# Optimization experiments

Hardware: AMD Instinct MI355X
Metric: run time of the kernel (lower is better)

Reference implementation:

```python
import jax, jax.numpy as jnp
import numpy as np

B, S, HID = 2, 2048, 4096
NUM_HEADS, NUM_KV_HEADS, HEAD_DIM = 32, 8, 128
KV_SIZE = HID * NUM_KV_HEADS // NUM_HEADS  # 1024


def setup_inputs() -> dict:
    key = jax.random.key(0)
    ks = jax.random.split(key, 5)
    x = jax.random.normal(ks[0], (B, S, HID), dtype=jnp.float32)
    wq = jax.random.normal(ks[1], (HID, HID), dtype=jnp.float32) * 0.02
    wk = jax.random.normal(ks[2], (HID, KV_SIZE), dtype=jnp.float32) * 0.02
    wv = jax.random.normal(ks[3], (HID, KV_SIZE), dtype=jnp.float32) * 0.02
    wo = jax.random.normal(ks[4], (KV_SIZE, HID), dtype=jnp.float32) * 0.02
    return {"x": x, "wq": wq, "wk": wk, "wv": wv, "wo": wo}


def reference(x, wq, wk, wv, wo):
    b, s, _ = x.shape
    g = NUM_HEADS // NUM_KV_HEADS  # num_head_groups
    q = x @ wq  # [b, s, hid]
    k = x @ wk  # [b, s, kv_size]
    v = x @ wv  # [b, s, kv_size]
    # 'b s (h d) -> b h s d' with h = num_heads
    q = q.reshape(b, s, NUM_HEADS, HEAD_DIM).transpose(0, 2, 1, 3)
    # 'b s (h d) -> b h d s' with h = num_kv_heads
    k = k.reshape(b, s, NUM_KV_HEADS, HEAD_DIM).transpose(0, 2, 3, 1)
    # 'b s (h d) -> b h s d'
    v = v.reshape(b, s, NUM_KV_HEADS, HEAD_DIM).transpose(0, 2, 1, 3)
    # 'b (h g) s d -> b g h s d' with g = num_head_groups, h = num_kv_heads
    q = q.reshape(b, NUM_KV_HEADS, g, s, HEAD_DIM).transpose(0, 2, 1, 3, 4)
    # NOTE: faithful to source - g is contracted (summed) here, it does not
    # appear in the output subscripts.
    scores = jnp.einsum('bghqd,bhdk->bhqk', q, k) / jnp.sqrt(
        jnp.asarray(HEAD_DIM, dtype=x.dtype))
    scores = jax.nn.softmax(scores, axis=-1)
    values = jnp.einsum('bhqk,bhkd->bhqd', scores, v)  # [b, h_kv, s, d]
    values = values.transpose(0, 2, 1, 3).reshape(b, s, KV_SIZE)
    return values @ wo  # [b, s, hid]
```

## Files before the change

kernel.cpp:

```cpp
#include <hip/hip_runtime.h>
#include <stdint.h>

#define S 2048
#define HID 4096
#define NKV 8
#define HD 128
#define KV 1024
#define BATCH 2
#define NQKV 3072
#define MROWS 4096

typedef __attribute__((ext_vector_type(4))) float f32x4;
typedef __attribute__((ext_vector_type(8))) __bf16 bf16x8;
typedef __attribute__((ext_vector_type(8))) unsigned short ushort8;
typedef __attribute__((ext_vector_type(4))) unsigned short ushort4_t;
typedef __attribute__((ext_vector_type(4))) float float4_t;

__device__ __forceinline__ unsigned short f2bf(float f) {
    unsigned int u = __builtin_bit_cast(unsigned int, f);
    u += 0x7fffu + ((u >> 16) & 1u);
    return (unsigned short)(u >> 16);
}
__device__ __forceinline__ float bf2f(unsigned short s) {
    unsigned int u = ((unsigned int)s) << 16;
    return __builtin_bit_cast(float, u);
}

__device__ __forceinline__ void gl2lds16(const void* g, void* l) {
    __builtin_amdgcn_global_load_lds(
        (const __attribute__((address_space(1))) void*)(uintptr_t)(g),
        (__attribute__((address_space(3))) void*)(uintptr_t)(l),
        16, 0, 0);
}

__global__ __launch_bounds__(256) void castx_kernel(const float* __restrict__ x,
                                                    unsigned short* __restrict__ xb) {
    int i = (blockIdx.x * 256 + threadIdx.x) * 4;
    float4_t v = *(const float4_t*)&x[i];
    ushort4_t o;
    o.x = f2bf(v.x); o.y = f2bf(v.y); o.z = f2bf(v.z); o.w = f2bf(v.w);
    *(ushort4_t*)&xb[i] = o;
}

__global__ __launch_bounds__(256) void wcat_kernel(const float* __restrict__ wq,
                                                   const float* __restrict__ wk,
                                                   const float* __restrict__ wv,
                                                   unsigned short* __restrict__ WcatT) {
    __shared__ float T[64 * 65];
    const int tid = threadIdx.x;
    const int k0 = blockIdx.x * 64;
    const int n0 = blockIdx.y * 64;
    const float scale = 0.088388347648318447f;
#pragma unroll
    for (int i = 0; i < 16; i++) {
        int kl = (tid >> 6) + i * 4;
        int nl = tid & 63;
        int k = k0 + kl, n = n0 + nl;
        float v;
        if (n < KV) {
            int kvh = n >> 7, d = n & 127;
            const float* p = wq + (size_t)k * HID + kvh * 512 + d;
            v = (p[0] + p[128] + p[256] + p[384]) * scale;
        } else if (n < 2048) {
            v = wk[(size_t)k * KV + (n - KV)];
        } else {
            v = wv[(size_t)k * KV + (n - 2048)];
        }
        T[kl * 65 + nl] = v;
    }
    __syncthreads();
#pragma unroll
    for (int i = 0; i < 16; i++) {
        int nl = (tid >> 6) + i * 4;
        int kl = tid & 63;
        WcatT[(size_t)(n0 + nl) * HID + k0 + kl] = f2bf(T[kl * 65 + nl]);
    }
}

__global__ __launch_bounds__(256) void wot_kernel(const float* __restrict__ wo,
                                                  unsigned short* __restrict__ woT) {
    __shared__ float T[64 * 65];
    const int tid = threadIdx.x;
    const int k0 = blockIdx.x * 64;
    const int n0 = blockIdx.y * 64;
#pragma unroll
    for (int i = 0; i < 16; i++) {
        int kl = (tid >> 6) + i * 4, nl = tid & 63;
        T[kl * 65 + nl] = wo[(size_t)(k0 + kl) * HID + n0 + nl];
    }
    __syncthreads();
#pragma unroll
    for (int i = 0; i < 16; i++) {
        int nl = (tid >> 6) + i * 4, kl = tid & 63;
        woT[(size_t)(n0 + nl) * KV + k0 + kl] = f2bf(T[kl * 65 + nl]);
    }
}

#define SBAR() __builtin_amdgcn_s_barrier()
#define SCHED0() __builtin_amdgcn_sched_barrier(0)
#define WAITV6() asm volatile("s_waitcnt vmcnt(6)")

template <int OUT_BF16>
__global__ __launch_bounds__(512, 2) void gemm_bt8(const unsigned short* __restrict__ A,
                                                   const unsigned short* __restrict__ Bt,
                                                   void* __restrict__ Cv,
                                                   int M, int N, int K) {
    __shared__ unsigned short As[2][2][8192];
    __shared__ unsigned short Bs[2][2][8192];
    const int tid = threadIdx.x;
    const int lane = tid & 63, wave = tid >> 6;
    const int lm = lane & 15, quad = lane >> 4;
    const int wm = wave >> 2;
    const int wn = wave & 3;
    const int wnh = wn >> 1;
    const int wnb = (wn & 1) * 4;

    const int nbx = gridDim.x;
    const int id = blockIdx.y * nbx + blockIdx.x;
    const int cpx = (nbx * gridDim.y) >> 3;
    const int sid = (id & 7) * cpx + (id >> 3);
    const int m0 = (sid / nbx) * 256;
    const int n0 = (sid % nbx) * 256;

    size_t so0, so1;
    {
#pragma unroll
        for (int i = 0; i < 2; i++) {
            int p = i * 512 + tid;
            int ps = p ^ (((p >> 5) & 1) << 1);
            int s = ps >> 6, w = ps & 63;
            int row = ((s >> 1) << 4) + (w >> 2);
            int kc = ((s & 1) << 5) + ((w & 3) << 3);
            size_t off = (size_t)row * K + kc;
            if (i == 0) so0 = off; else so1 = off;
        }
    }
    const unsigned short* Agb = A + (size_t)m0 * K;
    const unsigned short* Bgb = Bt + (size_t)n0 * K;
    const size_t hK = (size_t)128 * K;

#define STLO(G, L) gl2lds16((G) + so0, (L) + (size_t)tid * 8)
#define STHI(G, L) gl2lds16((G) + so1, (L) + (size_t)(512 + tid) * 8)

    const int roff = lm * 32 + ((quad << 3) ^ (((lm >> 3) & 1) << 4));

#define LDA(mi, kk, BUF) a[(mi) & 3][kk] = *(const bf16x8*)&As[BUF][wm][(((mi) * 2 + (kk)) << 9) + roff]
#define LDB(ni, kk, BUF) b[ni][kk] = *(const bf16x8*)&Bs[BUF][wnh][(((wnb + (ni)) * 2 + (kk)) << 9) + roff]
#define RD_A_LO(BUF) { LDA(0,0,BUF); LDA(0,1,BUF); LDA(1,0,BUF); LDA(1,1,BUF); LDA(2,0,BUF); LDA(2,1,BUF); LDA(3,0,BUF); LDA(3,1,BUF); }
#define RD_A_HI(BUF) { LDA(4,0,BUF); LDA(4,1,BUF); LDA(5,0,BUF); LDA(5,1,BUF); LDA(6,0,BUF); LDA(6,1,BUF); LDA(7,0,BUF); LDA(7,1,BUF); }
#define RD_B_LO(BUF) { LDB(0,0,BUF); LDB(0,1,BUF); LDB(1,0,BUF); LDB(1,1,BUF); }
#define RD_B_HI(BUF) { LDB(2,0,BUF); LDB(2,1,BUF); LDB(3,0,BUF); LDB(3,1,BUF); }
#define MFMA_Q(MB, NB) do { \
    __builtin_amdgcn_s_setprio(1); \
    _Pragma("unroll") for (int i_ = 0; i_ < 4; i_++) \
    _Pragma("unroll") for (int j_ = 0; j_ < 2; j_++) \
    _Pragma("unroll") for (int k_ = 0; k_ < 2; k_++) \
        acc[(MB) + i_][(NB) + j_] = __builtin_amdgcn_mfma_f32_16x16x32_bf16( \
            a[i_][k_], b[(NB) + j_][k_], acc[(MB) + i_][(NB) + j_], 0, 0, 0); \
    __builtin_amdgcn_s_setprio(0); \
} while (0)

    f32x4 acc[8][4] = {};
    bf16x8 a[4][2], b[4][2];

    const int KT = K >> 6;
    const int NT = KT >> 1;

    STLO(Agb, &As[0][0][0]); STLO(Agb + hK, &As[0][1][0]);
    STHI(Agb, &As[0][0][0]); STHI(Agb + hK, &As[0][1][0]);
    STLO(Bgb, &Bs[0][0][0]); STLO(Bgb + hK, &Bs[0][1][0]);
    STHI(Bgb, &Bs[0][0][0]); STHI(Bgb + hK, &Bs[0][1][0]);
    STLO(Agb + 64, &As[1][0][0]); STLO(Agb + hK + 64, &As[1][1][0]);
    STLO(Bgb + 64, &Bs[1][0][0]); STLO(Bgb + hK + 64, &Bs[1][1][0]);
    STHI(Bgb + 64, &Bs[1][0][0]); STHI(Bgb + hK + 64, &Bs[1][1][0]);
    WAITV6();
    SCHED0();
    SBAR();

    for (int t = 0; t < NT; ++t) {
        const size_t k1 = (size_t)(2 * t + 1) * 64;
        int t2i = 2 * t + 2; if (t2i >= KT) t2i = KT - 1;
        int t3i = 2 * t + 3; if (t3i >= KT) t3i = KT - 1;
        const size_t k2 = (size_t)t2i * 64, k3 = (size_t)t3i * 64;

        RD_A_LO(0); RD_B_LO(0);
        STHI(Agb + k1, &As[1][0][0]); STHI(Agb + hK + k1, &As[1][1][0]);
        SCHED0(); SBAR(); MFMA_Q(0, 0); SBAR();

        RD_B_HI(0);
        STLO(Agb + k2, &As[0][0][0]); STLO(Agb + hK + k2, &As[0][1][0]);
        SCHED0(); SBAR(); MFMA_Q(0, 2); SBAR();

        RD_A_HI(0);
        STLO(Bgb + k2, &Bs[0][0][0]); STLO(Bgb + hK + k2, &Bs[0][1][0]);
        SCHED0(); SBAR(); MFMA_Q(4, 2); SBAR();

        STHI(Bgb + k2, &Bs[0][0][0]); STHI(Bgb + hK + k2, &Bs[0][1][0]);
        SCHED0(); SBAR(); MFMA_Q(4, 0);
        WAITV6();
        SCHED0();
        SBAR();

        RD_A_LO(1); RD_B_LO(1);
        STHI(Agb + k2, &As[0][0][0]); STHI(Agb + hK + k2, &As[0][1][0]);
        SCHED0(); SBAR(); MFMA_Q(0, 0); SBAR();

        RD_B_HI(1);
        STLO(Agb + k3, &As[1][0][0]); STLO(Agb + hK + k3, &As[1][1][0]);
        SCHED0(); SBAR(); MFMA_Q(0, 2); SBAR();

        RD_A_HI(1);
        STLO(Bgb + k3, &Bs[1][0][0]); STLO(Bgb + hK + k3, &Bs[1][1][0]);
        SCHED0(); SBAR(); MFMA_Q(4, 2); SBAR();

        STHI(Bgb + k3, &Bs[1][0][0]); STHI(Bgb + hK + k3, &Bs[1][1][0]);
        SCHED0(); SBAR(); MFMA_Q(4, 0);
        WAITV6();
        SCHED0();
        SBAR();
    }

    const int crow0 = m0 + wm * 128 + quad * 4;
    const int ccol0 = n0 + wn * 64 + lm;
#pragma unroll
    for (int mi = 0; mi < 8; mi++)
#pragma unroll
        for (int ni = 0; ni < 4; ni++)
#pragma unroll
            for (int r = 0; r < 4; r++) {
                const int row = crow0 + mi * 16 + r;
                const int col = ccol0 + ni * 16;
                if (OUT_BF16)
                    ((unsigned short*)Cv)[(size_t)row * N + col] = f2bf(acc[mi][ni][r]);
                else
                    ((float*)Cv)[(size_t)row * N + col] = acc[mi][ni][r];
            }
#undef LDA
#undef LDB
#undef RD_A_LO
#undef RD_A_HI
#undef RD_B_LO
#undef RD_B_HI
#undef MFMA_Q
#undef STLO
#undef STHI
}

__global__ __launch_bounds__(256) void vt_kernel(const unsigned short* __restrict__ QKV,
                                                 unsigned short* __restrict__ Vt) {
    __shared__ unsigned short T[128 * 136];
    const int tid = threadIdx.x;
    const int st = blockIdx.x;
    const int bh = blockIdx.y;
    const int b = bh >> 3, h = bh & 7;
#pragma unroll
    for (int it = 0; it < 8; it++) {
        int chunk = tid + it * 256;
        int s = chunk >> 4, cc = chunk & 15;
        ushort8 v = *(const ushort8*)&QKV[(size_t)(b * S + st * 128 + s) * NQKV + 2048 + h * HD + cc * 8];
        *(ushort8*)&T[s * 136 + cc * 8] = v;
    }
    __syncthreads();
#pragma unroll
    for (int it = 0; it < 8; it++) {
        int chunk = tid + it * 256;
        int d = chunk >> 4, scc = chunk & 15;
        ushort8 o;
#pragma unroll
        for (int j = 0; j < 8; j++) o[j] = T[(scc * 8 + j) * 136 + d];
        *(ushort8*)&Vt[(size_t)((b * NKV + h) * HD + d) * S + st * 128 + scc * 8] = o;
    }
}

__global__ __launch_bounds__(256, 2) void attn_kernel(const unsigned short* __restrict__ QKV,
                                                      const unsigned short* __restrict__ Vt,
                                                      unsigned short* __restrict__ Oout) {
    __shared__ unsigned short Ks[64 * 128];
    __shared__ unsigned short Vs[128 * 64];
    __shared__ unsigned short Ps[64 * 64];
    const int tid = threadIdx.x;
    const int lane = tid & 63, wave = tid >> 6;
    const int lm = lane & 15, quad = lane >> 4;
    const int sw = lm & 7;
    const int h = blockIdx.x;
    const int qt = blockIdx.y;
    const int b = blockIdx.z;
    const int qrow0 = qt * 64 + wave * 16;

    bf16x8 qf[4];
#pragma unroll
    for (int ks = 0; ks < 4; ks++) {
        size_t off = (size_t)(b * S + qrow0 + lm) * NQKV + h * HD + ks * 32 + quad * 8;
        qf[ks] = *(const bf16x8*)&QKV[off];
    }

    float lsum[4] = {};
    f32x4 oacc[8] = {};

    const int krow = tid >> 2, kc4 = tid & 3;
    const int vrow = tid >> 1, vc2 = tid & 1;
    const unsigned short* Kg0 = QKV + (size_t)(b * S) * NQKV + KV + h * HD + kc4 * 32;
    const unsigned short* Vg0 = Vt + (size_t)((b * NKV + h) * HD + vrow) * S + vc2 * 32;

    ushort8 kreg[4], vreg[4];
    {
        const unsigned short* kg = Kg0 + (size_t)krow * NQKV;
        const unsigned short* vg = Vg0;
#pragma unroll
        for (int j = 0; j < 4; j++) kreg[j] = *(const ushort8*)(kg + j * 8);
#pragma unroll
        for (int j = 0; j < 4; j++) vreg[j] = *(const ushort8*)(vg + j * 8);
    }

    for (int kt = 0; kt < 32; kt++) {
        __syncthreads();
#pragma unroll
        for (int j = 0; j < 4; j++)
            *(ushort8*)&Ks[krow * 128 + ((kc4 * 4 + j) ^ (krow & 7)) * 8] = kreg[j];
#pragma unroll
        for (int j = 0; j < 4; j++)
            *(ushort8*)&Vs[vrow * 64 + ((vc2 * 4 + j) ^ (vrow & 7)) * 8] = vreg[j];
        __syncthreads();
        if (kt < 31) {
            const unsigned short* kg = Kg0 + (size_t)((kt + 1) * 64 + krow) * NQKV;
            const unsigned short* vg = Vg0 + (kt + 1) * 64;
#pragma unroll
            for (int j = 0; j < 4; j++) kreg[j] = *(const ushort8*)(kg + j * 8);
#pragma unroll
            for (int j = 0; j < 4; j++) vreg[j] = *(const ushort8*)(vg + j * 8);
        }

        f32x4 sc[4] = {};
#pragma unroll
        for (int ks = 0; ks < 4; ks++)
#pragma unroll
            for (int ct = 0; ct < 4; ct++) {
                bf16x8 kf = *(const bf16x8*)&Ks[(ct * 16 + lm) * 128 + ((ks * 4 + quad) ^ sw) * 8];
                sc[ct] = __builtin_amdgcn_mfma_f32_16x16x32_bf16(qf[ks], kf, sc[ct], 0, 0, 0);
            }

#pragma unroll
        for (int ct = 0; ct < 4; ct++)
#pragma unroll
            for (int r = 0; r < 4; r++) {
                float p = __expf(fminf(sc[ct][r], 60.f));
                unsigned short pb = f2bf(p);
                lsum[r] += bf2f(pb);
                int prow = wave * 16 + quad * 4 + r;
                int pcol = ct * 16 + lm;
                Ps[prow * 64 + (((pcol >> 3) ^ (prow & 7)) * 8) + (pcol & 7)] = pb;
            }

#pragma unroll
        for (int ks = 0; ks < 2; ks++) {
            bf16x8 af = *(const bf16x8*)&Ps[(wave * 16 + lm) * 64 + ((ks * 4 + quad) ^ sw) * 8];
#pragma unroll
            for (int dt = 0; dt < 8; dt++) {
                bf16x8 vf = *(const bf16x8*)&Vs[(dt * 16 + lm) * 64 + ((ks * 4 + quad) ^ sw) * 8];
                oacc[dt] = __builtin_amdgcn_mfma_f32_16x16x32_bf16(af, vf, oacc[dt], 0, 0, 0);
            }
        }
    }

#pragma unroll
    for (int r = 0; r < 4; r++) {
        float v = lsum[r];
        v += __shfl_xor(v, 8);
        v += __shfl_xor(v, 4);
        v += __shfl_xor(v, 2);
        v += __shfl_xor(v, 1);
        lsum[r] = v;
    }
#pragma unroll
    for (int dt = 0; dt < 8; dt++)
#pragma unroll
        for (int r = 0; r < 4; r++) {
            int row = b * S + qt * 64 + wave * 16 + quad * 4 + r;
            int col = h * HD + dt * 16 + lm;
            Oout[(size_t)row * KV + col] = f2bf(oacc[dt][r] / lsum[r]);
        }
}

extern "C" void kernel_launch(void* const* d_in, const int* in_sizes, int n_in,
                              void* d_out, int out_size, void* d_ws, size_t ws_size,
                              hipStream_t stream) {
    (void)in_sizes; (void)n_in; (void)out_size; (void)ws_size;
    const float* x  = (const float*)d_in[0];
    const float* wq = (const float*)d_in[1];
    const float* wk = (const float*)d_in[2];
    const float* wv = (const float*)d_in[3];
    const float* wo = (const float*)d_in[4];
    float* out = (float*)d_out;
    char* ws = (char*)d_ws;

    unsigned short* xb    = (unsigned short*)(ws);
    unsigned short* WcatT = (unsigned short*)(ws + 33554432);
    unsigned short* woT   = (unsigned short*)(ws + 33554432 + 25165824);
    unsigned short* QKV   = (unsigned short*)(ws + 67108864);
    unsigned short* Vt    = (unsigned short*)(ws);
    unsigned short* AttnO = (unsigned short*)(ws + 8388608);

    castx_kernel<<<16384, 256, 0, stream>>>(x, xb);
    wcat_kernel<<<dim3(64, 48), 256, 0, stream>>>(wq, wk, wv, WcatT);
    wot_kernel<<<dim3(16, 64), 256, 0, stream>>>(wo, woT);
    gemm_bt8<1><<<dim3(NQKV / 256, MROWS / 256), 512, 0, stream>>>(xb, WcatT, QKV, MROWS, NQKV, HID);
    vt_kernel<<<dim3(16, 16), 256, 0, stream>>>(QKV, Vt);
    attn_kernel<<<dim3(NKV, 32, BATCH), 256, 0, stream>>>(QKV, Vt, AttnO);
    gemm_bt8<0><<<dim3(HID / 256, MROWS / 256), 512, 0, stream>>>(AttnO, woT, out, MROWS, HID, KV);
}
```

Baseline: 427.1 us.

## Fuse V transpose into QKV GEMM epilogue and prefetch LDS fragments earlier

The QKV GEMM gains an output mode that writes the V columns directly in transposed [b,h,d,s] layout as bf16. When the workspace is large enough this replaces the separate vt_kernel launch and its extra read/write of V. The GEMM main loop is also reorganised: B fragments are split into two register sets and the A/B LDS reads for the next quarter are issued before the barrier or after the MFMAs, so LDS latency overlaps compute. The transposed stores are 8-byte strided writes, which may coalesce poorly, and the extra fragment registers raise register pressure.

```diff
diff --git a/kernel.cpp b/kernel.cpp
--- a/kernel.cpp
+++ b/kernel.cpp
@@ -100,10 +100,11 @@
 #define SCHED0() __builtin_amdgcn_sched_barrier(0)
 #define WAITV6() asm volatile("s_waitcnt vmcnt(6)")
 
-template <int OUT_BF16>
+template <int OUT_MODE>
 __global__ __launch_bounds__(512, 2) void gemm_bt8(const unsigned short* __restrict__ A,
                                                    const unsigned short* __restrict__ Bt,
                                                    void* __restrict__ Cv,
+                                                   unsigned short* __restrict__ VtT,
                                                    int M, int N, int K) {
     __shared__ unsigned short As[2][2][8192];
     __shared__ unsigned short Bs[2][2][8192];
@@ -144,24 +145,26 @@
 
     const int roff = lm * 32 + ((quad << 3) ^ (((lm >> 3) & 1) << 4));
 
-#define LDA(mi, kk, BUF) a[(mi) & 3][kk] = *(const bf16x8*)&As[BUF][wm][(((mi) * 2 + (kk)) << 9) + roff]
-#define LDB(ni, kk, BUF) b[ni][kk] = *(const bf16x8*)&Bs[BUF][wnh][(((wnb + (ni)) * 2 + (kk)) << 9) + roff]
-#define RD_A_LO(BUF) { LDA(0,0,BUF); LDA(0,1,BUF); LDA(1,0,BUF); LDA(1,1,BUF); LDA(2,0,BUF); LDA(2,1,BUF); LDA(3,0,BUF); LDA(3,1,BUF); }
-#define RD_A_HI(BUF) { LDA(4,0,BUF); LDA(4,1,BUF); LDA(5,0,BUF); LDA(5,1,BUF); LDA(6,0,BUF); LDA(6,1,BUF); LDA(7,0,BUF); LDA(7,1,BUF); }
-#define RD_B_LO(BUF) { LDB(0,0,BUF); LDB(0,1,BUF); LDB(1,0,BUF); LDB(1,1,BUF); }
-#define RD_B_HI(BUF) { LDB(2,0,BUF); LDB(2,1,BUF); LDB(3,0,BUF); LDB(3,1,BUF); }
-#define MFMA_Q(MB, NB) do { \
+#define RA(mi, kk, BUF) (*(const bf16x8*)&As[BUF][wm][(((mi) * 2 + (kk)) << 9) + roff])
+#define RB(ni, kk, BUF) (*(const bf16x8*)&Bs[BUF][wnh][(((wnb + (ni)) * 2 + (kk)) << 9) + roff])
+#define RD_A_LO_K0(BUF) { a[0][0]=RA(0,0,BUF); a[1][0]=RA(1,0,BUF); a[2][0]=RA(2,0,BUF); a[3][0]=RA(3,0,BUF); }
+#define RD_A_LO_K1(BUF) { a[0][1]=RA(0,1,BUF); a[1][1]=RA(1,1,BUF); a[2][1]=RA(2,1,BUF); a[3][1]=RA(3,1,BUF); }
+#define RD_A_HI(BUF)    { a[0][0]=RA(4,0,BUF); a[0][1]=RA(4,1,BUF); a[1][0]=RA(5,0,BUF); a[1][1]=RA(5,1,BUF); \
+                          a[2][0]=RA(6,0,BUF); a[2][1]=RA(6,1,BUF); a[3][0]=RA(7,0,BUF); a[3][1]=RA(7,1,BUF); }
+#define RD_BN(BUF) { bn[0][0]=RB(0,0,BUF); bn[0][1]=RB(0,1,BUF); bn[1][0]=RB(1,0,BUF); bn[1][1]=RB(1,1,BUF); }
+#define RD_BH(BUF) { bh[0][0]=RB(2,0,BUF); bh[0][1]=RB(2,1,BUF); bh[1][0]=RB(3,0,BUF); bh[1][1]=RB(3,1,BUF); }
+#define MFMA_Q(MB, NB, BB) do { \
     __builtin_amdgcn_s_setprio(1); \
     _Pragma("unroll") for (int i_ = 0; i_ < 4; i_++) \
     _Pragma("unroll") for (int j_ = 0; j_ < 2; j_++) \
     _Pragma("unroll") for (int k_ = 0; k_ < 2; k_++) \
         acc[(MB) + i_][(NB) + j_] = __builtin_amdgcn_mfma_f32_16x16x32_bf16( \
-            a[i_][k_], b[(NB) + j_][k_], acc[(MB) + i_][(NB) + j_], 0, 0, 0); \
+            a[i_][k_], BB[j_][k_], acc[(MB) + i_][(NB) + j_], 0, 0, 0); \
     __builtin_amdgcn_s_setprio(0); \
 } while (0)
 
     f32x4 acc[8][4] = {};
-    bf16x8 a[4][2], b[4][2];
+    bf16x8 a[4][2], bn[2][2], bh[2][2];
 
     const int KT = K >> 6;
     const int NT = KT >> 1;
@@ -175,6 +178,7 @@
     STHI(Bgb + 64, &Bs[1][0][0]); STHI(Bgb + hK + 64, &Bs[1][1][0]);
     WAITV6();
     SCHED0();
+    RD_A_LO_K0(0); RD_BN(0);
     SBAR();
 
     for (int t = 0; t < NT; ++t) {
@@ -183,64 +187,78 @@
         int t3i = 2 * t + 3; if (t3i >= KT) t3i = KT - 1;
         const size_t k2 = (size_t)t2i * 64, k3 = (size_t)t3i * 64;
 
-        RD_A_LO(0); RD_B_LO(0);
+        RD_A_LO_K1(0); RD_BH(0);
         STHI(Agb + k1, &As[1][0][0]); STHI(Agb + hK + k1, &As[1][1][0]);
-        SCHED0(); SBAR(); MFMA_Q(0, 0); SBAR();
-
-        RD_B_HI(0);
+        SCHED0(); SBAR(); MFMA_Q(0, 0, bn); SBAR();
+
         STLO(Agb + k2, &As[0][0][0]); STLO(Agb + hK + k2, &As[0][1][0]);
-        SCHED0(); SBAR(); MFMA_Q(0, 2); SBAR();
-
-        RD_A_HI(0);
+        SCHED0(); SBAR(); MFMA_Q(0, 2, bh); RD_A_HI(0); SBAR();
+
         STLO(Bgb + k2, &Bs[0][0][0]); STLO(Bgb + hK + k2, &Bs[0][1][0]);
-        SCHED0(); SBAR(); MFMA_Q(4, 2); SBAR();
+        SCHED0(); SBAR(); MFMA_Q(4, 2, bh); SBAR();
 
         STHI(Bgb + k2, &Bs[0][0][0]); STHI(Bgb + hK + k2, &Bs[0][1][0]);
-        SCHED0(); SBAR(); MFMA_Q(4, 0);
-        WAITV6();
-        SCHED0();
+        SCHED0(); SBAR(); MFMA_Q(4, 0, bn);
+        WAITV6(); SCHED0();
+        RD_A_LO_K0(1); RD_BN(1);
         SBAR();
 
-        RD_A_LO(1); RD_B_LO(1);
+        RD_A_LO_K1(1); RD_BH(1);
         STHI(Agb + k2, &As[0][0][0]); STHI(Agb + hK + k2, &As[0][1][0]);
-        SCHED0(); SBAR(); MFMA_Q(0, 0); SBAR();
-
-        RD_B_HI(1);
+        SCHED0(); SBAR(); MFMA_Q(0, 0, bn); SBAR();
+
         STLO(Agb + k3, &As[1][0][0]); STLO(Agb + hK + k3, &As[1][1][0]);
-        SCHED0(); SBAR(); MFMA_Q(0, 2); SBAR();
-
-        RD_A_HI(1);
+        SCHED0(); SBAR(); MFMA_Q(0, 2, bh); RD_A_HI(1); SBAR();
+
         STLO(Bgb + k3, &Bs[1][0][0]); STLO(Bgb + hK + k3, &Bs[1][1][0]);
-        SCHED0(); SBAR(); MFMA_Q(4, 2); SBAR();
+        SCHED0(); SBAR(); MFMA_Q(4, 2, bh); SBAR();
 
         STHI(Bgb + k3, &Bs[1][0][0]); STHI(Bgb + hK + k3, &Bs[1][1][0]);
-        SCHED0(); SBAR(); MFMA_Q(4, 0);
-        WAITV6();
-        SCHED0();
+        SCHED0(); SBAR(); MFMA_Q(4, 0, bn);
+        WAITV6(); SCHED0();
+        RD_A_LO_K0(0); RD_BN(0);
         SBAR();
     }
 
     const int crow0 = m0 + wm * 128 + quad * 4;
     const int ccol0 = n0 + wn * 64 + lm;
-#pragma unroll
-    for (int mi = 0; mi < 8; mi++)
-#pragma unroll
-        for (int ni = 0; ni < 4; ni++)
-#pragma unroll
-            for (int r = 0; r < 4; r++) {
-                const int row = crow0 + mi * 16 + r;
-                const int col = ccol0 + ni * 16;
-                if (OUT_BF16)
-                    ((unsigned short*)Cv)[(size_t)row * N + col] = f2bf(acc[mi][ni][r]);
-                else
-                    ((float*)Cv)[(size_t)row * N + col] = acc[mi][ni][r];
+    if (OUT_MODE == 2 && n0 >= 2048) {
+        const int bb = crow0 >> 11;
+        const int s0 = crow0 & 2047;
+        const int dbase = (n0 - 2048) + wn * 64;
+#pragma unroll
+        for (int mi = 0; mi < 8; mi++)
+#pragma unroll
+            for (int ni = 0; ni < 4; ni++) {
+                int dcol = dbase + ni * 16 + lm;
+                int hh = dcol >> 7, dd = dcol & 127;
+                ushort4_t o;
+#pragma unroll
+                for (int r = 0; r < 4; r++) o[r] = f2bf(acc[mi][ni][r]);
+                *(ushort4_t*)&VtT[(size_t)((bb * NKV + hh) * HD + dd) * S + s0 + mi * 16] = o;
             }
-#undef LDA
-#undef LDB
-#undef RD_A_LO
+    } else {
+#pragma unroll
+        for (int mi = 0; mi < 8; mi++)
+#pragma unroll
+            for (int ni = 0; ni < 4; ni++)
+#pragma unroll
+                for (int r = 0; r < 4; r++) {
+                    const int row = crow0 + mi * 16 + r;
+                    const int col = ccol0 + ni * 16;
+                    if (OUT_MODE == 0)
+                        ((float*)Cv)[(size_t)row * N + col] = acc[mi][ni][r];
+                    else
+                        ((unsigned short*)Cv)[(size_t)row * N + col] = f2bf(acc[mi][ni][r]);
+                }
+    }
+#undef RA
+#undef RB
+#undef RD_A_LO_K0
+#undef RD_A_LO_K1
 #undef RD_A_HI
-#undef RD_B_LO
-#undef RD_B_HI
+#undef RD_BN
+#undef RD_BH
 #undef MFMA_Q
 #undef STLO
 #undef STHI
@@ -384,7 +402,7 @@
 extern "C" void kernel_launch(void* const* d_in, const int* in_sizes, int n_in,
                               void* d_out, int out_size, void* d_ws, size_t ws_size,
                               hipStream_t stream) {
-    (void)in_sizes; (void)n_in; (void)out_size; (void)ws_size;
+    (void)in_sizes; (void)n_in; (void)out_size;
     const float* x  = (const float*)d_in[0];
     const float* wq = (const float*)d_in[1];
     const float* wk = (const float*)d_in[2];
@@ -397,14 +415,22 @@
     unsigned short* WcatT = (unsigned short*)(ws + 33554432);
     unsigned short* woT   = (unsigned short*)(ws + 33554432 + 25165824);
     unsigned short* QKV   = (unsigned short*)(ws + 67108864);
-    unsigned short* Vt    = (unsigned short*)(ws);
     unsigned short* AttnO = (unsigned short*)(ws + 8388608);
+
+    const size_t VT_OFF = 67108864ull + 25165824ull;
+    const int fuse_vt = (ws_size >= VT_OFF + 8388608ull);
+    unsigned short* Vt = fuse_vt ? (unsigned short*)(ws + VT_OFF)
+                                 : (unsigned short*)(ws);
 
     castx_kernel<<<16384, 256, 0, stream>>>(x, xb);
     wcat_kernel<<<dim3(64, 48), 256, 0, stream>>>(wq, wk, wv, WcatT);
     wot_kernel<<<dim3(16, 64), 256, 0, stream>>>(wo, woT);
-    gemm_bt8<1><<<dim3(NQKV / 256, MROWS / 256), 512, 0, stream>>>(xb, WcatT, QKV, MROWS, NQKV, HID);
-    vt_kernel<<<dim3(16, 16), 256, 0, stream>>>(QKV, Vt);
+    if (fuse_vt) {
+        gemm_bt8<2><<<dim3(NQKV / 256, MROWS / 256), 512, 0, stream>>>(xb, WcatT, QKV, Vt, MROWS, NQKV, HID);
+    } else {
+        gemm_bt8<1><<<dim3(NQKV / 256, MROWS / 256), 512, 0, stream>>>(xb, WcatT, QKV, nullptr, MROWS, NQKV, HID);
+        vt_kernel<<<dim3(16, 16), 256, 0, stream>>>(QKV, Vt);
+    }
     attn_kernel<<<dim3(NKV, 32, BATCH), 256, 0, stream>>>(QKV, Vt, AttnO);
-    gemm_bt8<0><<<dim3(HID / 256, MROWS / 256), 512, 0, stream>>>(AttnO, woT, out, MROWS, HID, KV);
-}
+    gemm_bt8<0><<<dim3(HID / 256, MROWS / 256), 512, 0, stream>>>(AttnO, woT, out, nullptr, MROWS, HID, KV);
+}
```

Result: faster. 416.6 us (-2.5%).
